# Kernel optimization log

Hardware: AMD Instinct MI355X
Metric: run time of the kernel (lower is better)

Reference implementation:

```python
import jax, jax.numpy as jnp
import numpy as np

B, P, NP, D, DS, M, K = 2, 4000, 4096, 64, 64, 512, 8
NX, NY = 432, 496
HW = NY * NX


def _per_batch(points, pillars, pillars_scale, idx, W):
    # points: [NP, D], pillars: [P, D], pillars_scale: [P, DS], idx: [P] in [0, HW)
    # --- get_score: top-k point attention per pillar ---
    score = jax.nn.softmax(points @ pillars.T, axis=0)                # [NP, P], softmax over points
    top_idx = jax.lax.top_k(jax.lax.stop_gradient(score).T, K)[1]     # [P, K]
    pts_pos = points[top_idx]                                         # [P, K, D]
    agg = jax.nn.softmax(jnp.einsum('pd,pkd->pk', pillars, pts_pos), axis=1)
    pos_point = jnp.einsum('pk,pkd->pd', jax.lax.stop_gradient(agg), pts_pos)  # [P, D]
    # --- memory unit: top-k memory-item attention per pillar ---
    att = jax.nn.softmax(pillars @ W.T, axis=1)                       # [P, M]
    midx = jax.lax.top_k(jax.lax.stop_gradient(att), K)[1]            # [P, K]
    mem_pos = W[midx]                                                 # [P, K, D]
    magg = jax.nn.softmax(jnp.einsum('pd,pkd->pk', pillars, mem_pos), axis=1)
    pos_mem = jnp.einsum('pk,pkd->pd', magg, mem_pos)                 # [P, D]
    # --- scatter into dense BEV grids ---
    sp_point = jnp.zeros((2 * D, HW), pillars.dtype).at[:, idx].set(
        jnp.concatenate([pillars, pos_point], axis=1).T)
    sp = jnp.zeros((2 * D, HW), pillars.dtype).at[:, idx].set(
        jnp.concatenate([jax.lax.stop_gradient(pillars), pos_mem], axis=1).T)
    sp_scale = jnp.zeros((DS, HW), pillars_scale.dtype).at[:, idx].set(pillars_scale.T)
    return sp, sp_point, sp_scale, pos_point, pos_mem


def setup_inputs() -> dict:
    key = jax.random.key(0)
    k1, k2, k3, k4, k5 = jax.random.split(key, 5)
    return {
        'pillar_features': jax.random.normal(k1, (B, P, D), jnp.float32),
        'pillar_scale_features': jax.random.normal(k2, (B, P, DS), jnp.float32),
        'point_features': jax.random.normal(k3, (B, NP, D), jnp.float32),
        'memory_weight': jax.random.normal(k4, (M, D), jnp.float32),
        'indices': jax.random.randint(k5, (B, P), 0, HW, jnp.int32),
    }


def reference(pillar_features, pillar_scale_features, point_features, memory_weight, indices):
    sp, sp_point, sp_scale, pos_point, pos_mem = jax.vmap(
        _per_batch, in_axes=(0, 0, 0, 0, None))(
        point_features, pillar_features, pillar_scale_features, indices, memory_weight)
    spatial_features = sp.reshape(B, 2 * D, NY, NX)
    spatial_features_point = sp_point.reshape(B, 2 * D, NY, NX)
    spatial_scale_features = sp_scale.reshape(B, DS, NY, NX)
    point_positive_features = pos_point.reshape(B * P, D)
    memory_positive_features = pos_mem.reshape(B * P, D)
    return (spatial_features, spatial_features_point, spatial_scale_features,
            point_positive_features, memory_positive_features)
```

## Files before the change

### kernel.cpp

```cpp
#include <hip/hip_runtime.h>

#define B_     2
#define P_TOT  4000
#define NP_TOT 4096
#define D_     64
#define M_     512
#define HW_TOT 214272
#define J4     53568

#define O0 0UL
#define O1 54853632UL
#define O2 109707264UL
#define O3 137134080UL
#define O4 137646080UL

typedef __attribute__((ext_vector_type(8))) short bb8;
typedef __attribute__((ext_vector_type(4))) float f32x4;

__device__ __forceinline__ void fma4(float4& a, const float4& x, const float4& y) {
  a.x = fmaf(x.x, y.x, a.x);
  a.y = fmaf(x.y, y.y, a.y);
  a.z = fmaf(x.z, y.z, a.z);
  a.w = fmaf(x.w, y.w, a.w);
}

__device__ __forceinline__ void insert8(float sc, int n, float s[8], int ix[8]) {
  float cs = sc; int ci = n;
#pragma unroll
  for (int i = 0; i < 8; ++i) {
    bool gt = cs > s[i];
    float ts = s[i]; int ti = ix[i];
    s[i]  = gt ? cs : ts;  ix[i] = gt ? ci : ti;
    cs    = gt ? ts : cs;  ci    = gt ? ti : ci;
  }
}

__device__ __forceinline__ void split_bf16(float x, short& h, short& l) {
  unsigned fb = __float_as_uint(x);
  unsigned hb = fb & 0xFFFF0000u;
  float lof = x - __uint_as_float(hb);
  h = (short)(hb >> 16);
  l = (short)(__float_as_uint(lof) >> 16);
}

__global__ __launch_bounds__(256) void prep(
    const float* __restrict__ points, short* __restrict__ hi, short* __restrict__ lo,
    const int* __restrict__ indices, int* __restrict__ owner)
{
  if (blockIdx.x < 512) {
    int t = blockIdx.x * 256 + threadIdx.x;
    float4 v = ((const float4*)points)[t];
    float x[4] = {v.x, v.y, v.z, v.w};
    short h[4], l[4];
#pragma unroll
    for (int j = 0; j < 4; ++j) split_bf16(x[j], h[j], l[j]);
    ((short4*)hi)[t] = make_short4(h[0], h[1], h[2], h[3]);
    ((short4*)lo)[t] = make_short4(l[0], l[1], l[2], l[3]);
  } else {
    int t = (blockIdx.x - 512) * 256 + threadIdx.x;
    if (t >= B_ * P_TOT) return;
    int b = (t >= P_TOT) ? 1 : 0;
    int p = t - b * P_TOT;
    atomicMax(&owner[b * HW_TOT + indices[t]], p);
  }
}

__global__ __launch_bounds__(256) void topk_all(
    const float* __restrict__ pillars,
    const short* __restrict__ phi, const short* __restrict__ plo,
    const float* __restrict__ W,
    float* __restrict__ ws_pts_sc, int* __restrict__ ws_pts_ix,
    float* __restrict__ ws_mem_sc, int* __restrict__ ws_mem_ix)
{
  __shared__ float lds_pts[4224];
  __shared__ int   ci_lds[2080];

  const int tid = threadIdx.x;

  if (blockIdx.x < 1008) {
    const unsigned u = blockIdx.x;
    const int pt = u % 63, ch = (u / 63) % 8, b = u / 504;
    const int lane = tid & 63, wv = tid >> 6;
    const int sub = lane & 15, quad = lane >> 4;

    int prow = pt * 64 + wv * 16 + sub;
    if (prow >= P_TOT) prow = P_TOT - 1;
    const float* ap = pillars + ((size_t)(b * P_TOT) + prow) * D_;
    bb8 Ah0, Ah1, Al0, Al1;
    {
      const float4* a4 = (const float4*)(ap + quad * 8);
      const float4* b4 = (const float4*)(ap + 32 + quad * 8);
      float4 t0 = a4[0], t1 = a4[1], t2 = b4[0], t3 = b4[1];
      float av[16] = {t0.x, t0.y, t0.z, t0.w, t1.x, t1.y, t1.z, t1.w,
                      t2.x, t2.y, t2.z, t2.w, t3.x, t3.y, t3.z, t3.w};
#pragma unroll
      for (int j = 0; j < 8; ++j) {
        short h, l;
        split_bf16(av[j], h, l);     Ah0[j] = h; Al0[j] = l;
        split_bf16(av[8 + j], h, l); Ah1[j] = h; Al1[j] = l;
      }
    }

    float sv[4][8]; int iv[4][8];
#pragma unroll
    for (int r = 0; r < 4; ++r)
#pragma unroll
      for (int k = 0; k < 8; ++k) { sv[r][k] = -1e30f; iv[r][k] = 0; }

    const size_t bofs = ((size_t)(b * NP_TOT) + ch * 512) * D_;
    const short* bh = phi + bofs;
    const short* bl = plo + bofs;

#pragma unroll 2
    for (int it = 0; it < 32; ++it) {
      const int nr = it * 16 + sub;
      const short* rh = bh + nr * D_;
      const short* rl = bl + nr * D_;
      bb8 Bh0 = *(const bb8*)(rh + quad * 8);
      bb8 Bh1 = *(const bb8*)(rh + 32 + quad * 8);
      bb8 Bl0 = *(const bb8*)(rl + quad * 8);
      bb8 Bl1 = *(const bb8*)(rl + 32 + quad * 8);
      f32x4 acc = {0.f, 0.f, 0.f, 0.f};
      acc = __builtin_amdgcn_mfma_f32_16x16x32_bf16(Al0, Bh0, acc, 0, 0, 0);
      acc = __builtin_amdgcn_mfma_f32_16x16x32_bf16(Al1, Bh1, acc, 0, 0, 0);
      acc = __builtin_amdgcn_mfma_f32_16x16x32_bf16(Ah0, Bl0, acc, 0, 0, 0);
      acc = __builtin_amdgcn_mfma_f32_16x16x32_bf16(Ah1, Bl1, acc, 0, 0, 0);
      acc = __builtin_amdgcn_mfma_f32_16x16x32_bf16(Ah0, Bh0, acc, 0, 0, 0);
      acc = __builtin_amdgcn_mfma_f32_16x16x32_bf16(Ah1, Bh1, acc, 0, 0, 0);
      const int ng = ch * 512 + nr;
#pragma unroll
      for (int r = 0; r < 4; ++r) {
        float sc = acc[r];
        if (sc > sv[r][7]) insert8(sc, ng, sv[r], iv[r]);
      }
    }

    const int pbase = pt * 64 + wv * 16 + quad * 4;
#pragma unroll
    for (int r = 0; r < 4; ++r) {
      const int pg = pbase + r;
      float out_s = 0.f; int out_i = 0;
#pragma unroll
      for (int k = 0; k < 8; ++k) {
        unsigned fb = __float_as_uint(sv[r][0]);
        unsigned mk = (fb & 0x80000000u) ? ~fb : (fb | 0x80000000u);
        unsigned key = (mk & 0xFFFFFFF0u) | (unsigned)sub;
#pragma unroll
        for (int off = 1; off < 16; off <<= 1) {
          unsigned ok = (unsigned)__shfl_xor((int)key, off);
          key = key > ok ? key : ok;
        }
        const int wsub = (int)(key & 15u);
        const int wlane = (lane & 48) | wsub;
        float wsc = __shfl(sv[r][0], wlane);
        int   wix = __shfl(iv[r][0], wlane);
        if (sub == wsub) {
#pragma unroll
          for (int i2 = 0; i2 < 7; ++i2) { sv[r][i2] = sv[r][i2 + 1]; iv[r][i2] = iv[r][i2 + 1]; }
          sv[r][7] = -1e30f;
        }
        if (sub == k) { out_s = wsc; out_i = wix; }
      }
      if (sub < 8 && pg < P_TOT) {
        const size_t base = ((size_t)(b * P_TOT) + pg) * 64 + ch * 8 + sub;
        ws_pts_sc[base] = out_s; ws_pts_ix[base] = out_i;
      }
    }
  } else {
    const unsigned u = blockIdx.x - 1008;
    const int pt = u % 125, ch = (u / 125) % 8, b = u / 1000;
    const int pp = tid & 31, sg = tid >> 5;
    const int p = pt * 32 + pp;

    const float4* prow = (const float4*)(pillars + ((size_t)(b * P_TOT + p)) * D_);
    float4 pl[16];
#pragma unroll
    for (int i = 0; i < 16; ++i) pl[i] = prow[i];

    float s[8]; int ix[8];
#pragma unroll
    for (int i = 0; i < 8; ++i) { s[i] = -1e30f; ix[i] = 0; }

    const int n_base = ch * 64;
    const int r0 = tid >> 2, seg = tid & 3;

    {
      const float4* g = (const float4*)(W + ((size_t)(n_base + r0)) * D_ + seg * 16);
      float4* dst4 = (float4*)(lds_pts + r0 * 64 + seg * 16);
      dst4[0] = g[0]; dst4[1] = g[1]; dst4[2] = g[2]; dst4[3] = g[3];
      __syncthreads();

#pragma unroll
      for (int r = 0; r < 8; ++r) {
        const int row = sg * 8 + r;
        const float4* q = (const float4*)(lds_pts + row * 64);
        float4 a0 = {0,0,0,0}, a1 = {0,0,0,0}, a2 = {0,0,0,0}, a3 = {0,0,0,0};
#pragma unroll
        for (int i = 0; i < 4; ++i) {
          fma4(a0, pl[i*4+0], q[i*4+0]);
          fma4(a1, pl[i*4+1], q[i*4+1]);
          fma4(a2, pl[i*4+2], q[i*4+2]);
          fma4(a3, pl[i*4+3], q[i*4+3]);
        }
        float sc = ((a0.x + a1.x) + (a2.x + a3.x)) + ((a0.y + a1.y) + (a2.y + a3.y))
                 + ((a0.z + a1.z) + (a2.z + a3.z)) + ((a0.w + a1.w) + (a2.w + a3.w));
        int n = n_base + row;
        if (sc > s[7]) insert8(sc, n, s, ix);
      }
      __syncthreads();
    }

    float* cs_lds = lds_pts;
#pragma unroll
    for (int k = 0; k < 8; ++k) {
      cs_lds[pp * 65 + sg * 8 + k] = s[k];
      ci_lds[pp * 65 + sg * 8 + k] = ix[k];
    }
    __syncthreads();
    if (tid < 32) {
      float ms[8]; int mi[8];
#pragma unroll
      for (int i = 0; i < 8; ++i) { ms[i] = -1e30f; mi[i] = 0; }
      for (int k = 0; k < 64; ++k) {
        float sc = cs_lds[tid * 65 + k];
        int   ii = ci_lds[tid * 65 + k];
        if (sc > ms[7]) insert8(sc, ii, ms, mi);
      }
      const int p2 = pt * 32 + tid;
      size_t base = ((size_t)(b * P_TOT + p2)) * 64 + ch * 8;
#pragma unroll
      for (int k = 0; k < 8; ++k) { ws_mem_sc[base + k] = ms[k]; ws_mem_ix[base + k] = mi[k]; }
    }
  }
}

__global__ __launch_bounds__(256) void finalize2(
    const float* __restrict__ points, const float* __restrict__ W,
    const float* __restrict__ ws_sc_p, const int* __restrict__ ws_ix_p,
    const float* __restrict__ ws_sc_m, const int* __restrict__ ws_ix_m,
    float* __restrict__ out_p, float* __restrict__ out_m)
{
  const int tid = threadIdx.x;
  const int lane = tid & 63, wv = tid >> 6;
  const int gp = blockIdx.x * 4 + wv;
  const int b = (gp >= P_TOT) ? 1 : 0;
  const size_t cb = (size_t)gp * 64;
  const bool mem = (blockIdx.y == 1);

  const float* ws_sc = mem ? ws_sc_m : ws_sc_p;
  const int*   ws_ix = mem ? ws_ix_m : ws_ix_p;
  const float* sb    = mem ? W : (points + (size_t)b * (NP_TOT * D_));
  float*       outp  = mem ? out_m : out_p;

  float ss = ws_sc[cb + lane];
  const int myix = ws_ix[cb + lane];

  float wsc[8]; int wix[8];
#pragma unroll
  for (int k = 0; k < 8; ++k) {
    float cv = ss; int cl = lane;
#pragma unroll
    for (int off = 32; off >= 1; off >>= 1) {
      float ov = __shfl_xor(cv, off);
      int   ol = __shfl_xor(cl, off);
      if (ov > cv || (ov == cv && ol < cl)) { cv = ov; cl = ol; }
    }
    wsc[k] = cv;
    wix[k] = __shfl(myix, cl);
    if (lane == cl) ss = -1e30f;
  }

  const float m = wsc[0];
  float e[8], Z = 0.f;
#pragma unroll
  for (int k = 0; k < 8; ++k) { e[k] = expf(wsc[k] - m); Z += e[k]; }
  const float inv = 1.0f / Z;

  float acc = 0.f;
#pragma unroll
  for (int k = 0; k < 8; ++k)
    acc = fmaf(e[k] * inv, sb[(size_t)wix[k] * 64 + lane], acc);
  outp[cb + lane] = acc;
}

__global__ __launch_bounds__(256) void scatter5(
    const float* __restrict__ pillars, const float* __restrict__ scale,
    const float* __restrict__ pos_point, const float* __restrict__ pos_mem,
    const int* __restrict__ owner, float* __restrict__ out)
{
  const int j4 = blockIdx.x * 256 + threadIdx.x;
  if (j4 >= J4) return;
  const int c = blockIdx.y, b = blockIdx.z;

  const int4 own = ((const int4*)owner)[(size_t)b * J4 + j4];

  const size_t bo = (size_t)b * (P_TOT * D_);
  const float* sp = pillars   + bo;
  const float* sm = pos_mem   + bo;
  const float* sq = pos_point + bo;
  const float* ss = scale     + bo;

  f32x4 vp = {0.f, 0.f, 0.f, 0.f};
  f32x4 vm = vp, vq = vp, vs = vp;

  if ((own.x & own.y & own.z & own.w) >= 0) {
    const size_t rx = (size_t)(own.x < 0 ? 0 : own.x) * 64 + c;
    const size_t ry = (size_t)(own.y < 0 ? 0 : own.y) * 64 + c;
    const size_t rz = (size_t)(own.z < 0 ? 0 : own.z) * 64 + c;
    const size_t rw = (size_t)(own.w < 0 ? 0 : own.w) * 64 + c;
    vp = (f32x4){own.x < 0 ? 0.f : sp[rx], own.y < 0 ? 0.f : sp[ry],
                 own.z < 0 ? 0.f : sp[rz], own.w < 0 ? 0.f : sp[rw]};
    vm = (f32x4){own.x < 0 ? 0.f : sm[rx], own.y < 0 ? 0.f : sm[ry],
                 own.z < 0 ? 0.f : sm[rz], own.w < 0 ? 0.f : sm[rw]};
    vq = (f32x4){own.x < 0 ? 0.f : sq[rx], own.y < 0 ? 0.f : sq[ry],
                 own.z < 0 ? 0.f : sq[rz], own.w < 0 ? 0.f : sq[rw]};
    vs = (f32x4){own.x < 0 ? 0.f : ss[rx], own.y < 0 ? 0.f : ss[ry],
                 own.z < 0 ? 0.f : ss[rz], own.w < 0 ? 0.f : ss[rw]};
  }

  f32x4* o4 = (f32x4*)out;
  __builtin_nontemporal_store(vp, o4 + (size_t)(b * 128 + c)       * J4 + j4);
  __builtin_nontemporal_store(vm, o4 + (size_t)(b * 128 + 64 + c)  * J4 + j4);
  __builtin_nontemporal_store(vp, o4 + 13713408UL + (size_t)(b * 128 + c)      * J4 + j4);
  __builtin_nontemporal_store(vq, o4 + 13713408UL + (size_t)(b * 128 + 64 + c) * J4 + j4);
  __builtin_nontemporal_store(vs, o4 + 27426816UL + (size_t)(b * 64 + c)       * J4 + j4);
}

extern "C" void kernel_launch(void* const* d_in, const int* in_sizes, int n_in,
                              void* d_out, int out_size, void* d_ws, size_t ws_size,
                              hipStream_t stream) {
  const float* pillars = (const float*)d_in[0];
  const float* scale   = (const float*)d_in[1];
  const float* points  = (const float*)d_in[2];
  const float* W       = (const float*)d_in[3];
  const int*   indices = (const int*)d_in[4];
  float* out = (float*)d_out;

  float* ws_pts_sc = (float*)d_ws;
  int*   ws_pts_ix = (int*)d_ws + 512000;
  float* ws_mem_sc = (float*)d_ws + 1024000;
  int*   ws_mem_ix = (int*)d_ws + 1536000;
  int*   owner     = (int*)d_ws + 2048000;
  short* phi       = (short*)((int*)d_ws + 2480000);
  short* plo       = (short*)((int*)d_ws + 2760000);

  (void)hipMemsetAsync(owner, 0xFF, (size_t)B_ * HW_TOT * sizeof(int), stream);

  prep<<<544, 256, 0, stream>>>(points, phi, plo, indices, owner);

  topk_all<<<3008, 256, 0, stream>>>(
      pillars, phi, plo, W, ws_pts_sc, ws_pts_ix, ws_mem_sc, ws_mem_ix);

  finalize2<<<dim3(2000, 2), 256, 0, stream>>>(
      points, W, ws_pts_sc, ws_pts_ix, ws_mem_sc, ws_mem_ix, out + O3, out + O4);

  scatter5<<<dim3(210, 64, 2), 256, 0, stream>>>(
      pillars, scale, out + O3, out + O4, owner, out);
}
```

Before: 702.0 us.

## Move memory-item top-k scoring to split-bf16 MFMA path

Pre-splits the memory weight matrix W into bf16 hi/lo halves inside the prep kernel. The FP32 FMA/LDS path for pillar-vs-memory scores, with its separate top-k merge, is replaced by the same MFMA-based scoring and shuffle top-k used for points. Memory chunks use 4 MFMA products (lo*lo added) for extra precision. The aim is to cut the scalar FMA cost of the memory branch, at the risk of small ranking differences from bf16 splitting.

```diff
diff --git a/kernel.cpp b/kernel.cpp
--- a/kernel.cpp
+++ b/kernel.cpp
@@ -17,13 +17,6 @@
 typedef __attribute__((ext_vector_type(8))) short bb8;
 typedef __attribute__((ext_vector_type(4))) float f32x4;
 
-__device__ __forceinline__ void fma4(float4& a, const float4& x, const float4& y) {
-  a.x = fmaf(x.x, y.x, a.x);
-  a.y = fmaf(x.y, y.y, a.y);
-  a.z = fmaf(x.z, y.z, a.z);
-  a.w = fmaf(x.w, y.w, a.w);
-}
-
 __device__ __forceinline__ void insert8(float sc, int n, float s[8], int ix[8]) {
   float cs = sc; int ci = n;
 #pragma unroll
@@ -45,7 +38,8 @@
 
 __global__ __launch_bounds__(256) void prep(
     const float* __restrict__ points, short* __restrict__ hi, short* __restrict__ lo,
-    const int* __restrict__ indices, int* __restrict__ owner)
+    const int* __restrict__ indices, int* __restrict__ owner,
+    const float* __restrict__ W, short* __restrict__ whi, short* __restrict__ wlo)
 {
   if (blockIdx.x < 512) {
     int t = blockIdx.x * 256 + threadIdx.x;
@@ -56,180 +50,135 @@
     for (int j = 0; j < 4; ++j) split_bf16(x[j], h[j], l[j]);
     ((short4*)hi)[t] = make_short4(h[0], h[1], h[2], h[3]);
     ((short4*)lo)[t] = make_short4(l[0], l[1], l[2], l[3]);
-  } else {
+  } else if (blockIdx.x < 544) {
     int t = (blockIdx.x - 512) * 256 + threadIdx.x;
     if (t >= B_ * P_TOT) return;
     int b = (t >= P_TOT) ? 1 : 0;
     int p = t - b * P_TOT;
     atomicMax(&owner[b * HW_TOT + indices[t]], p);
-  }
-}
-
-__global__ __launch_bounds__(256) void topk_all(
+  } else {
+    int t = (blockIdx.x - 544) * 256 + threadIdx.x;
+    float4 v = ((const float4*)W)[t];
+    float x[4] = {v.x, v.y, v.z, v.w};
+    short h[4], l[4];
+#pragma unroll
+    for (int j = 0; j < 4; ++j) split_bf16(x[j], h[j], l[j]);
+    ((short4*)whi)[t] = make_short4(h[0], h[1], h[2], h[3]);
+    ((short4*)wlo)[t] = make_short4(l[0], l[1], l[2], l[3]);
+  }
+}
+
+__global__ __launch_bounds__(256) void topk_mfma(
     const float* __restrict__ pillars,
     const short* __restrict__ phi, const short* __restrict__ plo,
-    const float* __restrict__ W,
+    const short* __restrict__ whi, const short* __restrict__ wlo,
     float* __restrict__ ws_pts_sc, int* __restrict__ ws_pts_ix,
     float* __restrict__ ws_mem_sc, int* __restrict__ ws_mem_ix)
 {
-  __shared__ float lds_pts[4224];
-  __shared__ int   ci_lds[2080];
-
   const int tid = threadIdx.x;
-
-  if (blockIdx.x < 1008) {
-    const unsigned u = blockIdx.x;
-    const int pt = u % 63, ch = (u / 63) % 8, b = u / 504;
-    const int lane = tid & 63, wv = tid >> 6;
-    const int sub = lane & 15, quad = lane >> 4;
-
-    int prow = pt * 64 + wv * 16 + sub;
-    if (prow >= P_TOT) prow = P_TOT - 1;
-    const float* ap = pillars + ((size_t)(b * P_TOT) + prow) * D_;
-    bb8 Ah0, Ah1, Al0, Al1;
-    {
-      const float4* a4 = (const float4*)(ap + quad * 8);
-      const float4* b4 = (const float4*)(ap + 32 + quad * 8);
-      float4 t0 = a4[0], t1 = a4[1], t2 = b4[0], t3 = b4[1];
-      float av[16] = {t0.x, t0.y, t0.z, t0.w, t1.x, t1.y, t1.z, t1.w,
-                      t2.x, t2.y, t2.z, t2.w, t3.x, t3.y, t3.z, t3.w};
-#pragma unroll
-      for (int j = 0; j < 8; ++j) {
-        short h, l;
-        split_bf16(av[j], h, l);     Ah0[j] = h; Al0[j] = l;
-        split_bf16(av[8 + j], h, l); Ah1[j] = h; Al1[j] = l;
+  const int pt = blockIdx.x, chy = blockIdx.y, b = blockIdx.z;
+  const bool is_mem = chy >= 8;
+  const int ch = is_mem ? (chy - 8) : chy;
+  const int lane = tid & 63, wv = tid >> 6;
+  const int sub = lane & 15, quad = lane >> 4;
+
+  int prow = pt * 64 + wv * 16 + sub;
+  if (prow >= P_TOT) prow = P_TOT - 1;
+  const float* ap = pillars + ((size_t)(b * P_TOT) + prow) * D_;
+  bb8 Ah0, Ah1, Al0, Al1;
+  {
+    const float4* a4 = (const float4*)(ap + quad * 8);
+    const float4* b4 = (const float4*)(ap + 32 + quad * 8);
+    float4 t0 = a4[0], t1 = a4[1], t2 = b4[0], t3 = b4[1];
+    float av[16] = {t0.x, t0.y, t0.z, t0.w, t1.x, t1.y, t1.z, t1.w,
+                    t2.x, t2.y, t2.z, t2.w, t3.x, t3.y, t3.z, t3.w};
+#pragma unroll
+    for (int j = 0; j < 8; ++j) {
+      short h, l;
+      split_bf16(av[j], h, l);     Ah0[j] = h; Al0[j] = l;
+      split_bf16(av[8 + j], h, l); Ah1[j] = h; Al1[j] = l;
+    }
+  }
+
+  float sv[4][8]; int iv[4][8];
+#pragma unroll
+  for (int r = 0; r < 4; ++r)
+#pragma unroll
+    for (int k = 0; k < 8; ++k) { sv[r][k] = -1e30f; iv[r][k] = 0; }
+
+  const short* bh;
+  const short* bl;
+  int iters, ngb;
+  if (is_mem) {
+    bh = whi + (size_t)(ch * 64) * D_;
+    bl = wlo + (size_t)(ch * 64) * D_;
+    iters = 4;  ngb = ch * 64;
+  } else {
+    const size_t bofs = ((size_t)(b * NP_TOT) + ch * 512) * D_;
+    bh = phi + bofs;  bl = plo + bofs;
+    iters = 32; ngb = ch * 512;
+  }
+
+#pragma unroll 2
+  for (int it = 0; it < iters; ++it) {
+    const int nr = it * 16 + sub;
+    const short* rh = bh + nr * D_;
+    const short* rl = bl + nr * D_;
+    bb8 Bh0 = *(const bb8*)(rh + quad * 8);
+    bb8 Bh1 = *(const bb8*)(rh + 32 + quad * 8);
+    bb8 Bl0 = *(const bb8*)(rl + quad * 8);
+    bb8 Bl1 = *(const bb8*)(rl + 32 + quad * 8);
+    f32x4 acc = {0.f, 0.f, 0.f, 0.f};
+    if (is_mem) {
+      acc = __builtin_amdgcn_mfma_f32_16x16x32_bf16(Al0, Bl0, acc, 0, 0, 0);
+      acc = __builtin_amdgcn_mfma_f32_16x16x32_bf16(Al1, Bl1, acc, 0, 0, 0);
+    }
+    acc = __builtin_amdgcn_mfma_f32_16x16x32_bf16(Al0, Bh0, acc, 0, 0, 0);
+    acc = __builtin_amdgcn_mfma_f32_16x16x32_bf16(Al1, Bh1, acc, 0, 0, 0);
+    acc = __builtin_amdgcn_mfma_f32_16x16x32_bf16(Ah0, Bl0, acc, 0, 0, 0);
+    acc = __builtin_amdgcn_mfma_f32_16x16x32_bf16(Ah1, Bl1, acc, 0, 0, 0);
+    acc = __builtin_amdgcn_mfma_f32_16x16x32_bf16(Ah0, Bh0, acc, 0, 0, 0);
+    acc = __builtin_amdgcn_mfma_f32_16x16x32_bf16(Ah1, Bh1, acc, 0, 0, 0);
+    const int ng = ngb + nr;
+#pragma unroll
+    for (int r = 0; r < 4; ++r) {
+      float sc = acc[r];
+      if (sc > sv[r][7]) insert8(sc, ng, sv[r], iv[r]);
+    }
+  }
+
+  float* osc = is_mem ? ws_mem_sc : ws_pts_sc;
+  int*   oix = is_mem ? ws_mem_ix : ws_pts_ix;
+
+  const int pbase = pt * 64 + wv * 16 + quad * 4;
+#pragma unroll
+  for (int r = 0; r < 4; ++r) {
+    const int pg = pbase + r;
+    float out_s = 0.f; int out_i = 0;
+#pragma unroll
+    for (int k = 0; k < 8; ++k) {
+      unsigned fb = __float_as_uint(sv[r][0]);
+      unsigned mk = (fb & 0x80000000u) ? ~fb : (fb | 0x80000000u);
+      unsigned key = (mk & 0xFFFFFFF0u) | (unsigned)sub;
+#pragma unroll
+      for (int off = 1; off < 16; off <<= 1) {
+        unsigned ok = (unsigned)__shfl_xor((int)key, off);
+        key = key > ok ? key : ok;
       }
-    }
-
-    float sv[4][8]; int iv[4][8];
-#pragma unroll
-    for (int r = 0; r < 4; ++r)
-#pragma unroll
-      for (int k = 0; k < 8; ++k) { sv[r][k] = -1e30f; iv[r][k] = 0; }
-
-    const size_t bofs = ((size_t)(b * NP_TOT) + ch * 512) * D_;
-    const short* bh = phi + bofs;
-    const short* bl = plo + bofs;
-
-#pragma unroll 2
-    for (int it = 0; it < 32; ++it) {
-      const int nr = it * 16 + sub;
-      const short* rh = bh + nr * D_;
-      const short* rl = bl + nr * D_;
-      bb8 Bh0 = *(const bb8*)(rh + quad * 8);
-      bb8 Bh1 = *(const bb8*)(rh + 32 + quad * 8);
-      bb8 Bl0 = *(const bb8*)(rl + quad * 8);
-      bb8 Bl1 = *(const bb8*)(rl + 32 + quad * 8);
-      f32x4 acc = {0.f, 0.f, 0.f, 0.f};
-      acc = __builtin_amdgcn_mfma_f32_16x16x32_bf16(Al0, Bh0, acc, 0, 0, 0);
-      acc = __builtin_amdgcn_mfma_f32_16x16x32_bf16(Al1, Bh1, acc, 0, 0, 0);
-      acc = __builtin_amdgcn_mfma_f32_16x16x32_bf16(Ah0, Bl0, acc, 0, 0, 0);
-      acc = __builtin_amdgcn_mfma_f32_16x16x32_bf16(Ah1, Bl1, acc, 0, 0, 0);
-      acc = __builtin_amdgcn_mfma_f32_16x16x32_bf16(Ah0, Bh0, acc, 0, 0, 0);
-      acc = __builtin_amdgcn_mfma_f32_16x16x32_bf16(Ah1, Bh1, acc, 0, 0, 0);
-      const int ng = ch * 512 + nr;
-#pragma unroll
-      for (int r = 0; r < 4; ++r) {
-        float sc = acc[r];
-        if (sc > sv[r][7]) insert8(sc, ng, sv[r], iv[r]);
+      const int wsub = (int)(key & 15u);
+      const int wlane = (lane & 48) | wsub;
+      float wsc = __shfl(sv[r][0], wlane);
+      int   wix = __shfl(iv[r][0], wlane);
+      if (sub == wsub) {
+#pragma unroll
+        for (int i2 = 0; i2 < 7; ++i2) { sv[r][i2] = sv[r][i2 + 1]; iv[r][i2] = iv[r][i2 + 1]; }
+        sv[r][7] = -1e30f;
       }
-    }
-
-    const int pbase = pt * 64 + wv * 16 + quad * 4;
-#pragma unroll
-    for (int r = 0; r < 4; ++r) {
-      const int pg = pbase + r;
-      float out_s = 0.f; int out_i = 0;
-#pragma unroll
-      for (int k = 0; k < 8; ++k) {
-        unsigned fb = __float_as_uint(sv[r][0]);
-        unsigned mk = (fb & 0x80000000u) ? ~fb : (fb | 0x80000000u);
-        unsigned key = (mk & 0xFFFFFFF0u) | (unsigned)sub;
-#pragma unroll
-        for (int off = 1; off < 16; off <<= 1) {
-          unsigned ok = (unsigned)__shfl_xor((int)key, off);
-          key = key > ok ? key : ok;
-        }
-        const int wsub = (int)(key & 15u);
-        const int wlane = (lane & 48) | wsub;
-        float wsc = __shfl(sv[r][0], wlane);
-        int   wix = __shfl(iv[r][0], wlane);
-        if (sub == wsub) {
-#pragma unroll
-          for (int i2 = 0; i2 < 7; ++i2) { sv[r][i2] = sv[r][i2 + 1]; iv[r][i2] = iv[r][i2 + 1]; }
-          sv[r][7] = -1e30f;
-        }
-        if (sub == k) { out_s = wsc; out_i = wix; }
-      }
-      if (sub < 8 && pg < P_TOT) {
-        const size_t base = ((size_t)(b * P_TOT) + pg) * 64 + ch * 8 + sub;
-        ws_pts_sc[base] = out_s; ws_pts_ix[base] = out_i;
-      }
-    }
-  } else {
-    const unsigned u = blockIdx.x - 1008;
-    const int pt = u % 125, ch = (u / 125) % 8, b = u / 1000;
-    const int pp = tid & 31, sg = tid >> 5;
-    const int p = pt * 32 + pp;
-
-    const float4* prow = (const float4*)(pillars + ((size_t)(b * P_TOT + p)) * D_);
-    float4 pl[16];
-#pragma unroll
-    for (int i = 0; i < 16; ++i) pl[i] = prow[i];
-
-    float s[8]; int ix[8];
-#pragma unroll
-    for (int i = 0; i < 8; ++i) { s[i] = -1e30f; ix[i] = 0; }
-
-    const int n_base = ch * 64;
-    const int r0 = tid >> 2, seg = tid & 3;
-
-    {
-      const float4* g = (const float4*)(W + ((size_t)(n_base + r0)) * D_ + seg * 16);
-      float4* dst4 = (float4*)(lds_pts + r0 * 64 + seg * 16);
-      dst4[0] = g[0]; dst4[1] = g[1]; dst4[2] = g[2]; dst4[3] = g[3];
-      __syncthreads();
-
-#pragma unroll
-      for (int r = 0; r < 8; ++r) {
-        const int row = sg * 8 + r;
-        const float4* q = (const float4*)(lds_pts + row * 64);
-        float4 a0 = {0,0,0,0}, a1 = {0,0,0,0}, a2 = {0,0,0,0}, a3 = {0,0,0,0};
-#pragma unroll
-        for (int i = 0; i < 4; ++i) {
-          fma4(a0, pl[i*4+0], q[i*4+0]);
-          fma4(a1, pl[i*4+1], q[i*4+1]);
-          fma4(a2, pl[i*4+2], q[i*4+2]);
-          fma4(a3, pl[i*4+3], q[i*4+3]);
-        }
-        float sc = ((a0.x + a1.x) + (a2.x + a3.x)) + ((a0.y + a1.y) + (a2.y + a3.y))
-                 + ((a0.z + a1.z) + (a2.z + a3.z)) + ((a0.w + a1.w) + (a2.w + a3.w));
-        int n = n_base + row;
-        if (sc > s[7]) insert8(sc, n, s, ix);
-      }
-      __syncthreads();
-    }
-
-    float* cs_lds = lds_pts;
-#pragma unroll
-    for (int k = 0; k < 8; ++k) {
-      cs_lds[pp * 65 + sg * 8 + k] = s[k];
-      ci_lds[pp * 65 + sg * 8 + k] = ix[k];
-    }
-    __syncthreads();
-    if (tid < 32) {
-      float ms[8]; int mi[8];
-#pragma unroll
-      for (int i = 0; i < 8; ++i) { ms[i] = -1e30f; mi[i] = 0; }
-      for (int k = 0; k < 64; ++k) {
-        float sc = cs_lds[tid * 65 + k];
-        int   ii = ci_lds[tid * 65 + k];
-        if (sc > ms[7]) insert8(sc, ii, ms, mi);
-      }
-      const int p2 = pt * 32 + tid;
-      size_t base = ((size_t)(b * P_TOT + p2)) * 64 + ch * 8;
-#pragma unroll
-      for (int k = 0; k < 8; ++k) { ws_mem_sc[base + k] = ms[k]; ws_mem_ix[base + k] = mi[k]; }
+      if (sub == k) { out_s = wsc; out_i = wix; }
+    }
+    if (sub < 8 && pg < P_TOT) {
+      const size_t base = ((size_t)(b * P_TOT) + pg) * 64 + ch * 8 + sub;
+      osc[base] = out_s; oix[base] = out_i;
     }
   }
 }
@@ -343,13 +292,15 @@
   int*   owner     = (int*)d_ws + 2048000;
   short* phi       = (short*)((int*)d_ws + 2480000);
   short* plo       = (short*)((int*)d_ws + 2760000);
+  short* whi       = (short*)((int*)d_ws + 3030000);
+  short* wlo       = (short*)((int*)d_ws + 3050000);
 
   (void)hipMemsetAsync(owner, 0xFF, (size_t)B_ * HW_TOT * sizeof(int), stream);
 
-  prep<<<544, 256, 0, stream>>>(points, phi, plo, indices, owner);
-
-  topk_all<<<3008, 256, 0, stream>>>(
-      pillars, phi, plo, W, ws_pts_sc, ws_pts_ix, ws_mem_sc, ws_mem_ix);
+  prep<<<576, 256, 0, stream>>>(points, phi, plo, indices, owner, W, whi, wlo);
+
+  topk_mfma<<<dim3(63, 16, 2), 256, 0, stream>>>(
+      pillars, phi, plo, whi, wlo, ws_pts_sc, ws_pts_ix, ws_mem_sc, ws_mem_ix);
 
   finalize2<<<dim3(2000, 2), 256, 0, stream>>>(
       points, W, ws_pts_sc, ws_pts_ix, ws_mem_sc, ws_mem_ix, out + O3, out + O4);
```

Result: faster. 650.4 us (-7.3%).
